# Kernel tuning notes

Measured on AMD Instinct MI355X. Metric: run time of the kernel, lower is better.

## Reference

```python
import jax, jax.numpy as jnp
import numpy as np

INPUT_SIZE = 3072
CORE_SIZE = 1024
OUTPUT_SIZE = 100
BATCH = 8192


def _ri(key, shape, lo, hi):
    # small-range int8 values (torch rand*scale cast to int8)
    return jax.random.randint(key, shape, lo, hi, dtype=jnp.int32).astype(jnp.int8)


def setup_inputs() -> dict:
    key = jax.random.key(0)
    ks = jax.random.split(key, 14)
    return {
        # learned int8 weights (nonzero after EQI.apply updates)
        "W_itoc": _ri(ks[0], (INPUT_SIZE, CORE_SIZE), -3, 4),
        "W_itoc_b": _ri(ks[1], (CORE_SIZE,), -3, 4),
        "W_ctoc": _ri(ks[2], (CORE_SIZE, CORE_SIZE), -3, 4),
        "W_ctoc_b": _ri(ks[3], (CORE_SIZE,), -3, 4),
        "W_ctoo": _ri(ks[4], (CORE_SIZE, OUTPUT_SIZE), -3, 4),
        "W_ctoo_b": _ri(ks[5], (OUTPUT_SIZE,), -3, 4),
        # epsilon perturbations: EPSILON_SCALE=2 -> values in {-1,0,1}
        "e_itoc": _ri(ks[6], (INPUT_SIZE, CORE_SIZE), -2, 2),
        "e_itoc_b": _ri(ks[7], (CORE_SIZE,), -2, 2),
        "e_ctoc": _ri(ks[8], (CORE_SIZE, CORE_SIZE), -2, 2),
        "e_ctoc_b": _ri(ks[9], (CORE_SIZE,), -2, 2),
        "e_ctoo": _ri(ks[10], (CORE_SIZE, OUTPUT_SIZE), -2, 2),
        "e_ctoo_b": _ri(ks[11], (OUTPUT_SIZE,), -2, 2),
        # forward activations
        "inputs": _ri(ks[12], (BATCH, INPUT_SIZE), -4, 5),
        "hiddens": _ri(ks[13], (BATCH, CORE_SIZE), -4, 5),
    }


def _addmm_i8(x, w, b):
    # int8 addmm with wraparound semantics: accumulate in int32, cast back
    # to int8 (truncation == mod-256, matching torch int8 arithmetic).
    acc = jnp.matmul(x.astype(jnp.int32), w.astype(jnp.int32)) + b.astype(jnp.int32)
    return acc.astype(jnp.int8)


def reference(W_itoc, W_itoc_b, W_ctoc, W_ctoc_b, W_ctoo, W_ctoo_b,
              e_itoc, e_itoc_b, e_ctoc, e_ctoc_b, e_ctoo, e_ctoo_b,
              inputs, hiddens):
    # layer 1: inputs -> core (weight = W + epsilon, elementwise int8 add)
    i2c = _addmm_i8(inputs, W_itoc + e_itoc, W_itoc_b + e_itoc_b)      # [B, CORE]
    # layer 2: (hiddens + projected inputs) -> core
    h2 = _addmm_i8(hiddens + i2c, W_ctoc + e_ctoc, W_ctoc_b + e_ctoc_b)  # [B, CORE]
    # layer 3: core -> output
    out = _addmm_i8(h2, W_ctoo + e_ctoo, W_ctoo_b + e_ctoo_b)          # [B, OUT]
    return (h2, out)
```

## Files before the change

### kernel.cpp

```cpp
#include <hip/hip_runtime.h>

typedef int v4i  __attribute__((ext_vector_type(4)));
typedef int v16i __attribute__((ext_vector_type(16)));

__device__ __forceinline__ int pack4i(int a, int b, int c, int d) {
  return (a & 255) | ((b & 255) << 8) | ((c & 255) << 16) | ((d & 255) << 24);
}
__device__ __forceinline__ int badd4(int a, int b) {
  return ((a & 0x7f7f7f7f) + (b & 0x7f7f7f7f)) ^ ((a ^ b) & 0x80808080);
}

__device__ void pack_tile(const int* __restrict__ W, const int* __restrict__ E,
                          char* __restrict__ Bt, int K, int N,
                          int nx, int ky, char* lin) {
  const int t = threadIdx.x;
  const int n0 = nx * 64, k0 = ky * 256;
  {
    const int c  = t & 15;
    const int kq = t >> 4;
    const int ng = n0 + c * 4;
    #pragma unroll 4
    for (int s = 0; s < 16; ++s) {
      const int k = s * 16 + kq;
      const long grow = (long)(k0 + k) * N;
      int a0, a1, a2, a3;
      if (ng + 3 < N) {
        int4 wv = *(const int4*)(W + grow + ng);
        int4 ev = *(const int4*)(E + grow + ng);
        a0 = wv.x + ev.x; a1 = wv.y + ev.y; a2 = wv.z + ev.z; a3 = wv.w + ev.w;
      } else {
        a0 = (ng + 0 < N) ? W[grow + ng + 0] + E[grow + ng + 0] : 0;
        a1 = (ng + 1 < N) ? W[grow + ng + 1] + E[grow + ng + 1] : 0;
        a2 = (ng + 2 < N) ? W[grow + ng + 2] + E[grow + ng + 2] : 0;
        a3 = (ng + 3 < N) ? W[grow + ng + 3] + E[grow + ng + 3] : 0;
      }
      *(int*)(lin + k * 68 + c * 4) = pack4i(a0, a1, a2, a3);
    }
  }
  __syncthreads();
  {
    const int n = t & 63, kq = t >> 6;
    char* dst = Bt + (long)(n0 + n) * K + k0 + (kq << 6);
    int outv[16];
    #pragma unroll
    for (int g = 0; g < 16; ++g) {
      const int k = (kq << 6) + (g << 2);
      outv[g] = pack4i(lin[(k + 0) * 68 + n], lin[(k + 1) * 68 + n],
                       lin[(k + 2) * 68 + n], lin[(k + 3) * 68 + n]);
    }
    #pragma unroll
    for (int g = 0; g < 4; ++g)
      *(int4*)(dst + (g << 4)) =
          make_int4(outv[g * 4], outv[g * 4 + 1], outv[g * 4 + 2], outv[g * 4 + 3]);
  }
}

__global__ __launch_bounds__(256) void pack_weights_kernel(
    const int* W1, const int* E1, char* Bt1,
    const int* W2, const int* E2, char* Bt2,
    const int* W3, const int* E3, char* Bt3,
    const int* b1, const int* eb1, int* bs1,
    const int* b2, const int* eb2, int* bs2,
    const int* b3, const int* eb3, int* bs3) {
  __shared__ __align__(16) char smem[17408];
  const int bid = blockIdx.x;
  if (bid < 192) {
    pack_tile(W1, E1, Bt1, 3072, 1024, bid % 16, bid / 16, smem);
  } else if (bid < 256) {
    const int l = bid - 192;
    pack_tile(W2, E2, Bt2, 1024, 1024, l % 16, l / 16, smem);
  } else if (bid < 264) {
    const int l = bid - 256;
    pack_tile(W3, E3, Bt3, 1024, 100, l & 1, l >> 1, smem);
  } else {
    const int t = threadIdx.x;
    for (int i = t; i < 1024; i += 256) {
      bs1[i] = b1[i] + eb1[i];
      bs2[i] = b2[i] + eb2[i];
    }
    for (int i = t; i < 128; i += 256)
      bs3[i] = (i < 100) ? (b3[i] + eb3[i]) : 0;
  }
}

__global__ __launch_bounds__(256) void pack_copy_kernel(
    const int* __restrict__ X, char* __restrict__ X8,
    const int* __restrict__ H, char* __restrict__ H8) {
  const int bid = blockIdx.x;
  const int t = threadIdx.x;
  const int* __restrict__ src;
  char* __restrict__ dst;
  long base;
  if (bid < 768) { src = X; dst = X8; base = (long)bid * 32768; }
  else           { src = H; dst = H8; base = (long)(bid - 768) * 32768; }
  #pragma unroll 2
  for (int it = 0; it < 8; ++it) {
    const long o = base + (long)it * 4096 + t * 16;
    int4 a = *(const int4*)(src + o);
    int4 b = *(const int4*)(src + o + 4);
    int4 c = *(const int4*)(src + o + 8);
    int4 d = *(const int4*)(src + o + 12);
    *(int4*)(dst + o) = make_int4(pack4i(a.x, a.y, a.z, a.w),
                                  pack4i(b.x, b.y, b.z, b.w),
                                  pack4i(c.x, c.y, c.z, c.w),
                                  pack4i(d.x, d.y, d.z, d.w));
  }
}

template<int EPI>
__global__ __launch_bounds__(256, 4) void gemm_kernel(
    const char* __restrict__ A, const char* __restrict__ Btg,
    const int* __restrict__ bsum, const char* __restrict__ H8,
    char* __restrict__ A8out, int* __restrict__ Iout, const int K) {
  __shared__ __align__(16) char smem[30720];

  const int t = threadIdx.x;
  const int bid = blockIdx.x;
  const int mt = bid & 127, nt = bid >> 7;
  const long m0 = (long)mt << 6;
  const int n0 = nt << 7;

  const int lane = t & 63, w = t >> 6;
  const int lc = lane & 31, hg = lane >> 5;

  v16i acc[2] = {};

  const int am = t >> 2, ah = t & 3;
  const char* Arow = A + (m0 + am) * (long)K + ah * 16;
  const int aoff = am * 80 + ah * 16;
  const int bm = t >> 1, bh = t & 1;
  const char* Brow = Btg + (long)(n0 + bm) * K + bh * 32;
  const int boff = bm * 80 + bh * 32;

  const int abo = lc * 80 + hg * 16;
  const int bbo = (w * 32 + lc) * 80 + hg * 16;

  int4 ar, br0, br1;
  auto LOAD = [&](int kb) {
    ar  = *(const int4*)(Arow + kb);
    br0 = *(const int4*)(Brow + kb);
    br1 = *(const int4*)(Brow + kb + 16);
  };
  auto STORE = [&](int stage) {
    char* base = smem + stage * 15360;
    *(int4*)(base + aoff) = ar;
    *(int4*)(base + 5120 + boff)      = br0;
    *(int4*)(base + 5120 + boff + 16) = br1;
  };

  const int kiters = K >> 6;
  LOAD(0);
  STORE(0);
  __syncthreads();

  for (int kt = 0; kt < kiters; ++kt) {
    if (kt + 1 < kiters) LOAD((kt + 1) << 6);
    const char* base = smem + (kt & 1) * 15360;
    const char* Ab = base + abo;
    const char* Bb = base + 5120 + bbo;
    #pragma unroll
    for (int ks = 0; ks < 2; ++ks) {
      v4i a0 = *(const v4i*)(Ab + ks * 32);
      v4i a1 = *(const v4i*)(Ab + 32 * 80 + ks * 32);
      v4i b  = *(const v4i*)(Bb + ks * 32);
      acc[0] = __builtin_amdgcn_mfma_i32_32x32x32_i8(a0, b, acc[0], 0, 0, 0);
      acc[1] = __builtin_amdgcn_mfma_i32_32x32x32_i8(a1, b, acc[1], 0, 0, 0);
    }
    if (kt + 1 < kiters) {
      STORE((kt + 1) & 1);
      __syncthreads();
    }
  }

  const int gcl = w * 32 + lc;
  const int bs = bsum[n0 + gcl];
  if (EPI == 1) {
    #pragma unroll
    for (int tm = 0; tm < 2; ++tm) {
      #pragma unroll
      for (int r = 0; r < 16; ++r) {
        const int row = tm * 32 + (hg << 2) + (r & 3) + ((r >> 2) << 3);
        Iout[(m0 + row) * 1024 + n0 + gcl] = (int)(signed char)(acc[tm][r] + bs);
      }
    }
  } else {
    __syncthreads();
    #pragma unroll
    for (int tm = 0; tm < 2; ++tm) {
      #pragma unroll
      for (int r = 0; r < 16; ++r) {
        const int row = tm * 32 + (hg << 2) + (r & 3) + ((r >> 2) << 3);
        smem[row * 144 + gcl] = (char)(acc[tm][r] + bs);
      }
    }
    __syncthreads();
    const char* src = smem + (t >> 2) * 144 + (t & 3) * 32;
    const long gm = m0 + (t >> 2);
    const long gco = gm * 1024 + n0 + (t & 3) * 32;
    int4 s0 = *(const int4*)(src);
    int4 s1 = *(const int4*)(src + 16);
    int4 h0 = *(const int4*)(H8 + gco);
    int4 h1 = *(const int4*)(H8 + gco + 16);
    s0 = make_int4(badd4(s0.x, h0.x), badd4(s0.y, h0.y),
                   badd4(s0.z, h0.z), badd4(s0.w, h0.w));
    s1 = make_int4(badd4(s1.x, h1.x), badd4(s1.y, h1.y),
                   badd4(s1.z, h1.z), badd4(s1.w, h1.w));
    *(int4*)(A8out + gco)      = s0;
    *(int4*)(A8out + gco + 16) = s1;
  }
}

__global__ __launch_bounds__(256, 2) void gemm3_kernel(
    const int* __restrict__ h2, const char* __restrict__ Btg,
    const int* __restrict__ bsum, int* __restrict__ Iout) {
  __shared__ __align__(16) char smem[23040];
  const int t = threadIdx.x;
  const int m0 = blockIdx.x << 4;
  const int lane = t & 63, w = t >> 6;
  const int l16 = lane & 15, q = lane >> 4;
  v4i acc0 = {}, acc1 = {};

  const int am = t >> 4, ah = t & 15;
  const int* Arow = h2 + (long)(m0 + am) * 1024 + ah * 4;
  const int aoff = am * 80 + ah * 4;
  const int bm = t >> 1, bh = t & 1;
  const char* Brow = Btg + (long)bm * 1024 + bh * 32;
  const int boff = bm * 80 + bh * 32;

  const int abo  = l16 * 80 + q * 16;
  const int bbo0 = (w * 32 + l16) * 80 + q * 16;
  const int bbo1 = (w * 32 + 16 + l16) * 80 + q * 16;

  int4 ar, br0, br1;
  auto LOAD = [&](int kt) {
    const int kb = kt << 6;
    ar  = *(const int4*)(Arow + kb);
    br0 = *(const int4*)(Brow + kb);
    br1 = *(const int4*)(Brow + kb + 16);
  };
  auto STORE = [&](int stage) {
    char* base = smem + stage * 11520;
    *(int*)(base + aoff) = pack4i(ar.x, ar.y, ar.z, ar.w);
    *(int4*)(base + 1280 + boff)      = br0;
    *(int4*)(base + 1280 + boff + 16) = br1;
  };
  auto MFMA = [&](int stage) {
    const char* base = smem + stage * 11520;
    v4i a  = *(const v4i*)(base + abo);
    v4i b0 = *(const v4i*)(base + 1280 + bbo0);
    v4i b1 = *(const v4i*)(base + 1280 + bbo1);
    acc0 = __builtin_amdgcn_mfma_i32_16x16x64_i8(a, b0, acc0, 0, 0, 0);
    acc1 = __builtin_amdgcn_mfma_i32_16x16x64_i8(a, b1, acc1, 0, 0, 0);
  };

  LOAD(0); STORE(0); __syncthreads();
  for (int kt = 0; kt < 16; ++kt) {
    if (kt + 1 < 16) LOAD(kt + 1);
    MFMA(kt & 1);
    if (kt + 1 < 16) { STORE((kt + 1) & 1); __syncthreads(); }
  }

  const int c0 = w * 32 + l16;
  const int c1 = c0 + 16;
  if (c0 < 100) {
    const int b = bsum[c0];
    #pragma unroll
    for (int r = 0; r < 4; ++r)
      Iout[(long)(m0 + q * 4 + r) * 100 + c0] = (int)(signed char)(acc0[r] + b);
  }
  if (c1 < 100) {
    const int b = bsum[c1];
    #pragma unroll
    for (int r = 0; r < 4; ++r)
      Iout[(long)(m0 + q * 4 + r) * 100 + c1] = (int)(signed char)(acc1[r] + b);
  }
}

extern "C" void kernel_launch(void* const* d_in, const int* in_sizes, int n_in,
                              void* d_out, int out_size, void* d_ws, size_t ws_size,
                              hipStream_t stream) {
  (void)in_sizes; (void)n_in; (void)out_size; (void)ws_size;
  const int* W1  = (const int*)d_in[0];
  const int* b1  = (const int*)d_in[1];
  const int* W2  = (const int*)d_in[2];
  const int* b2  = (const int*)d_in[3];
  const int* W3  = (const int*)d_in[4];
  const int* b3  = (const int*)d_in[5];
  const int* E1  = (const int*)d_in[6];
  const int* eb1 = (const int*)d_in[7];
  const int* E2  = (const int*)d_in[8];
  const int* eb2 = (const int*)d_in[9];
  const int* E3  = (const int*)d_in[10];
  const int* eb3 = (const int*)d_in[11];
  const int* X   = (const int*)d_in[12];
  const int* H   = (const int*)d_in[13];
  int* out = (int*)d_out;

  char* ws  = (char*)d_ws;
  char* Bt1 = ws;
  char* Bt2 = Bt1 + 3145728;
  char* Bt3 = Bt2 + 1048576;
  int*  bs1 = (int*)(Bt3 + 131072);
  int*  bs2 = bs1 + 1024;
  int*  bs3 = bs2 + 1024;
  char* A2  = (char*)(bs3 + 128);
  char* X8  = (char*)d_out;
  char* H8  = X8 + 25165824;

  pack_weights_kernel<<<dim3(265), dim3(256), 0, stream>>>(
      W1, E1, Bt1, W2, E2, Bt2, W3, E3, Bt3,
      b1, eb1, bs1, b2, eb2, bs2, b3, eb3, bs3);

  pack_copy_kernel<<<dim3(1024), dim3(256), 0, stream>>>(X, X8, H, H8);

  gemm_kernel<0><<<dim3(1024), dim3(256), 0, stream>>>(
      X8, Bt1, bs1, H8, A2, nullptr, 3072);

  gemm_kernel<1><<<dim3(1024), dim3(256), 0, stream>>>(
      A2, Bt2, bs2, nullptr, nullptr, out, 1024);

  gemm3_kernel<<<dim3(512), dim3(256), 0, stream>>>(
      out, Bt3, bs3, out + 8388608);
}
```

Before: 312.9 us.

## Fuse int32-to-int8 activation packing into first GEMM and its epilogue

Removes the standalone pass that converted the int32 input and hidden activations to int8. The first GEMM now loads int32 X tiles, packs them into int8 while staging to shared memory, and packs H in the epilogue before the byte-wise add. This saves one kernel launch and the write and reread of the packed copies. In exchange, each X tile is fetched as int32 by every n-tile block, which quadruples A-operand bytes through the cache hierarchy and adds packing ALU work to the main loop.

Result: slower. 339.6 us (+8.6%).

```diff
diff --git a/kernel.cpp b/kernel.cpp
--- a/kernel.cpp
+++ b/kernel.cpp
@@ -83,35 +83,121 @@
   }
 }
 
-__global__ __launch_bounds__(256) void pack_copy_kernel(
-    const int* __restrict__ X, char* __restrict__ X8,
-    const int* __restrict__ H, char* __restrict__ H8) {
+__global__ __launch_bounds__(256, 4) void gemm1_kernel(
+    const int* __restrict__ X, const char* __restrict__ Btg,
+    const int* __restrict__ bsum, const int* __restrict__ H,
+    char* __restrict__ A8out) {
+  const int K = 3072;
+  __shared__ __align__(16) char smem[30720];
+
+  const int t = threadIdx.x;
   const int bid = blockIdx.x;
-  const int t = threadIdx.x;
-  const int* __restrict__ src;
-  char* __restrict__ dst;
-  long base;
-  if (bid < 768) { src = X; dst = X8; base = (long)bid * 32768; }
-  else           { src = H; dst = H8; base = (long)(bid - 768) * 32768; }
-  #pragma unroll 2
-  for (int it = 0; it < 8; ++it) {
-    const long o = base + (long)it * 4096 + t * 16;
-    int4 a = *(const int4*)(src + o);
-    int4 b = *(const int4*)(src + o + 4);
-    int4 c = *(const int4*)(src + o + 8);
-    int4 d = *(const int4*)(src + o + 12);
-    *(int4*)(dst + o) = make_int4(pack4i(a.x, a.y, a.z, a.w),
-                                  pack4i(b.x, b.y, b.z, b.w),
-                                  pack4i(c.x, c.y, c.z, c.w),
-                                  pack4i(d.x, d.y, d.z, d.w));
-  }
-}
-
-template<int EPI>
-__global__ __launch_bounds__(256, 4) void gemm_kernel(
+  const int mt = bid & 127, nt = bid >> 7;
+  const long m0 = (long)mt << 6;
+  const int n0 = nt << 7;
+
+  const int lane = t & 63, w = t >> 6;
+  const int lc = lane & 31, hg = lane >> 5;
+
+  v16i acc[2] = {};
+
+  const int am = t >> 2, ah = t & 3;
+  const int* Xrow = X + (m0 + am) * (long)K + ah * 16;
+  const int aoff = am * 80 + ah * 16;
+  const int bm = t >> 1, bh = t & 1;
+  const char* Brow = Btg + (long)(n0 + bm) * K + bh * 32;
+  const int boff = bm * 80 + bh * 32;
+
+  const int abo = lc * 80 + hg * 16;
+  const int bbo = (w * 32 + lc) * 80 + hg * 16;
+
+  int4 a0r, a1r, a2r, a3r, br0, br1;
+  auto LOAD = [&](int kb) {
+    const int* p = Xrow + kb;
+    a0r = *(const int4*)(p);
+    a1r = *(const int4*)(p + 4);
+    a2r = *(const int4*)(p + 8);
+    a3r = *(const int4*)(p + 12);
+    br0 = *(const int4*)(Brow + kb);
+    br1 = *(const int4*)(Brow + kb + 16);
+  };
+  auto STORE = [&](int stage) {
+    char* base = smem + stage * 15360;
+    *(int4*)(base + aoff) = make_int4(
+        pack4i(a0r.x, a0r.y, a0r.z, a0r.w),
+        pack4i(a1r.x, a1r.y, a1r.z, a1r.w),
+        pack4i(a2r.x, a2r.y, a2r.z, a2r.w),
+        pack4i(a3r.x, a3r.y, a3r.z, a3r.w));
+    *(int4*)(base + 5120 + boff)      = br0;
+    *(int4*)(base + 5120 + boff + 16) = br1;
+  };
+
+  const int kiters = K >> 6;
+  LOAD(0);
+  STORE(0);
+  __syncthreads();
+
+  for (int kt = 0; kt < kiters; ++kt) {
+    if (kt + 1 < kiters) LOAD((kt + 1) << 6);
+    const char* base = smem + (kt & 1) * 15360;
+    const char* Ab = base + abo;
+    const char* Bb = base + 5120 + bbo;
+    #pragma unroll
+    for (int ks = 0; ks < 2; ++ks) {
+      v4i a0 = *(const v4i*)(Ab + ks * 32);
+      v4i a1 = *(const v4i*)(Ab + 32 * 80 + ks * 32);
+      v4i b  = *(const v4i*)(Bb + ks * 32);
+      acc[0] = __builtin_amdgcn_mfma_i32_32x32x32_i8(a0, b, acc[0], 0, 0, 0);
+      acc[1] = __builtin_amdgcn_mfma_i32_32x32x32_i8(a1, b, acc[1], 0, 0, 0);
+    }
+    if (kt + 1 < kiters) {
+      STORE((kt + 1) & 1);
+      __syncthreads();
+    }
+  }
+
+  const int gcl = w * 32 + lc;
+  const int bs = bsum[n0 + gcl];
+  __syncthreads();
+  #pragma unroll
+  for (int tm = 0; tm < 2; ++tm) {
+    #pragma unroll
+    for (int r = 0; r < 16; ++r) {
+      const int row = tm * 32 + (hg << 2) + (r & 3) + ((r >> 2) << 3);
+      smem[row * 144 + gcl] = (char)(acc[tm][r] + bs);
+    }
+  }
+  __syncthreads();
+  const char* src = smem + (t >> 2) * 144 + (t & 3) * 32;
+  const long gm = m0 + (t >> 2);
+  const long gco = gm * 1024 + n0 + (t & 3) * 32;
+  const int* hp = H + gco;
+  int4 s0 = *(const int4*)(src);
+  int4 s1 = *(const int4*)(src + 16);
+  int4 h0 = *(const int4*)(hp);
+  int4 h1 = *(const int4*)(hp + 4);
+  int4 h2 = *(const int4*)(hp + 8);
+  int4 h3 = *(const int4*)(hp + 12);
+  int4 h4 = *(const int4*)(hp + 16);
+  int4 h5 = *(const int4*)(hp + 20);
+  int4 h6 = *(const int4*)(hp + 24);
+  int4 h7 = *(const int4*)(hp + 28);
+  s0 = make_int4(badd4(s0.x, pack4i(h0.x, h0.y, h0.z, h0.w)),
+                 badd4(s0.y, pack4i(h1.x, h1.y, h1.z, h1.w)),
+                 badd4(s0.z, pack4i(h2.x, h2.y, h2.z, h2.w)),
+                 badd4(s0.w, pack4i(h3.x, h3.y, h3.z, h3.w)));
+  s1 = make_int4(badd4(s1.x, pack4i(h4.x, h4.y, h4.z, h4.w)),
+                 badd4(s1.y, pack4i(h5.x, h5.y, h5.z, h5.w)),
+                 badd4(s1.z, pack4i(h6.x, h6.y, h6.z, h6.w)),
+                 badd4(s1.w, pack4i(h7.x, h7.y, h7.z, h7.w)));
+  *(int4*)(A8out + gco)      = s0;
+  *(int4*)(A8out + gco + 16) = s1;
+}
+
+__global__ __launch_bounds__(256, 4) void gemm2_kernel(
     const char* __restrict__ A, const char* __restrict__ Btg,
-    const int* __restrict__ bsum, const char* __restrict__ H8,
-    char* __restrict__ A8out, int* __restrict__ Iout, const int K) {
+    const int* __restrict__ bsum, int* __restrict__ Iout) {
+  const int K = 1024;
   __shared__ __align__(16) char smem[30720];
 
   const int t = threadIdx.x;
@@ -174,39 +260,13 @@
 
   const int gcl = w * 32 + lc;
   const int bs = bsum[n0 + gcl];
-  if (EPI == 1) {
-    #pragma unroll
-    for (int tm = 0; tm < 2; ++tm) {
-      #pragma unroll
-      for (int r = 0; r < 16; ++r) {
-        const int row = tm * 32 + (hg << 2) + (r & 3) + ((r >> 2) << 3);
-        Iout[(m0 + row) * 1024 + n0 + gcl] = (int)(signed char)(acc[tm][r] + bs);
-      }
-    }
-  } else {
-    __syncthreads();
-    #pragma unroll
-    for (int tm = 0; tm < 2; ++tm) {
-      #pragma unroll
-      for (int r = 0; r < 16; ++r) {
-        const int row = tm * 32 + (hg << 2) + (r & 3) + ((r >> 2) << 3);
-        smem[row * 144 + gcl] = (char)(acc[tm][r] + bs);
-      }
-    }
-    __syncthreads();
-    const char* src = smem + (t >> 2) * 144 + (t & 3) * 32;
-    const long gm = m0 + (t >> 2);
-    const long gco = gm * 1024 + n0 + (t & 3) * 32;
-    int4 s0 = *(const int4*)(src);
-    int4 s1 = *(const int4*)(src + 16);
-    int4 h0 = *(const int4*)(H8 + gco);
-    int4 h1 = *(const int4*)(H8 + gco + 16);
-    s0 = make_int4(badd4(s0.x, h0.x), badd4(s0.y, h0.y),
-                   badd4(s0.z, h0.z), badd4(s0.w, h0.w));
-    s1 = make_int4(badd4(s1.x, h1.x), badd4(s1.y, h1.y),
-                   badd4(s1.z, h1.z), badd4(s1.w, h1.w));
-    *(int4*)(A8out + gco)      = s0;
-    *(int4*)(A8out + gco + 16) = s1;
+  #pragma unroll
+  for (int tm = 0; tm < 2; ++tm) {
+    #pragma unroll
+    for (int r = 0; r < 16; ++r) {
+      const int row = tm * 32 + (hg << 2) + (r & 3) + ((r >> 2) << 3);
+      Iout[(m0 + row) * 1024 + n0 + gcl] = (int)(signed char)(acc[tm][r] + bs);
+    }
   }
 }
 
@@ -304,20 +364,14 @@
   int*  bs2 = bs1 + 1024;
   int*  bs3 = bs2 + 1024;
   char* A2  = (char*)(bs3 + 128);
-  char* X8  = (char*)d_out;
-  char* H8  = X8 + 25165824;
 
   pack_weights_kernel<<<dim3(265), dim3(256), 0, stream>>>(
       W1, E1, Bt1, W2, E2, Bt2, W3, E3, Bt3,
       b1, eb1, bs1, b2, eb2, bs2, b3, eb3, bs3);
 
-  pack_copy_kernel<<<dim3(1024), dim3(256), 0, stream>>>(X, X8, H, H8);
-
-  gemm_kernel<0><<<dim3(1024), dim3(256), 0, stream>>>(
-      X8, Bt1, bs1, H8, A2, nullptr, 3072);
-
-  gemm_kernel<1><<<dim3(1024), dim3(256), 0, stream>>>(
-      A2, Bt2, bs2, nullptr, nullptr, out, 1024);
+  gemm1_kernel<<<dim3(1024), dim3(256), 0, stream>>>(X, Bt1, bs1, H, A2);
+
+  gemm2_kernel<<<dim3(1024), dim3(256), 0, stream>>>(A2, Bt2, bs2, out);
 
   gemm3_kernel<<<dim3(512), dim3(256), 0, stream>>>(
       out, Bt3, bs3, out + 8388608);
```

## Fuse int32-to-int8 input packing into GEMM1 and enlarge GEMM tiles to 128x256

Applied to the files above, without the earlier changes.

Removes the separate pack_copy kernel: GEMM1 now reads the int32 inputs directly and packs them to int8 while staging to shared memory, and packs the int32 hiddens in its epilogue. Both large GEMMs switch to 512-thread blocks with 128x256 output tiles (2x2 MFMA per wave) and a two-register-set prefetch scheme. This saves one full pass writing and re-reading packed activations and raises per-block data reuse. In exchange GEMM1 reads 4x more bytes of A per K-step from global memory, and the grid shrinks to 256 blocks, which may underfill the 256 CUs with 2 blocks per CU allowed.

Measured after the change: 310.6 us. No clear change (-0.7%).

```diff
diff --git a/kernel.cpp b/kernel.cpp
--- a/kernel.cpp
+++ b/kernel.cpp
@@ -83,130 +83,218 @@
   }
 }
 
-__global__ __launch_bounds__(256) void pack_copy_kernel(
-    const int* __restrict__ X, char* __restrict__ X8,
-    const int* __restrict__ H, char* __restrict__ H8) {
-  const int bid = blockIdx.x;
-  const int t = threadIdx.x;
-  const int* __restrict__ src;
-  char* __restrict__ dst;
-  long base;
-  if (bid < 768) { src = X; dst = X8; base = (long)bid * 32768; }
-  else           { src = H; dst = H8; base = (long)(bid - 768) * 32768; }
-  #pragma unroll 2
-  for (int it = 0; it < 8; ++it) {
-    const long o = base + (long)it * 4096 + t * 16;
-    int4 a = *(const int4*)(src + o);
-    int4 b = *(const int4*)(src + o + 4);
-    int4 c = *(const int4*)(src + o + 8);
-    int4 d = *(const int4*)(src + o + 12);
-    *(int4*)(dst + o) = make_int4(pack4i(a.x, a.y, a.z, a.w),
-                                  pack4i(b.x, b.y, b.z, b.w),
-                                  pack4i(c.x, c.y, c.z, c.w),
-                                  pack4i(d.x, d.y, d.z, d.w));
-  }
-}
-
-template<int EPI>
-__global__ __launch_bounds__(256, 4) void gemm_kernel(
-    const char* __restrict__ A, const char* __restrict__ Btg,
-    const int* __restrict__ bsum, const char* __restrict__ H8,
-    char* __restrict__ A8out, int* __restrict__ Iout, const int K) {
-  __shared__ __align__(16) char smem[30720];
-
+#define MFMA_I8(a, b, c) __builtin_amdgcn_mfma_i32_32x32x32_i8(a, b, c, 0, 0, 0)
+
+__global__ __launch_bounds__(512, 2) void gemm1_kernel(
+    const int* __restrict__ X, const char* __restrict__ Btg,
+    const int* __restrict__ bsum, const int* __restrict__ H,
+    char* __restrict__ A8out) {
+  const int K = 3072;
+  __shared__ __align__(16) char smem[61440];
   const int t = threadIdx.x;
   const int bid = blockIdx.x;
-  const int mt = bid & 127, nt = bid >> 7;
-  const long m0 = (long)mt << 6;
-  const int n0 = nt << 7;
+  const int mt = bid & 63, nt = bid >> 6;
+  const long m0 = (long)mt << 7;
+  const int n0 = nt << 8;
 
   const int lane = t & 63, w = t >> 6;
   const int lc = lane & 31, hg = lane >> 5;
-
-  v16i acc[2] = {};
-
-  const int am = t >> 2, ah = t & 3;
-  const char* Arow = A + (m0 + am) * (long)K + ah * 16;
-  const int aoff = am * 80 + ah * 16;
-  const int bm = t >> 1, bh = t & 1;
-  const char* Brow = Btg + (long)(n0 + bm) * K + bh * 32;
-  const int boff = bm * 80 + bh * 32;
-
-  const int abo = lc * 80 + hg * 16;
-  const int bbo = (w * 32 + lc) * 80 + hg * 16;
-
-  int4 ar, br0, br1;
-  auto LOAD = [&](int kb) {
-    ar  = *(const int4*)(Arow + kb);
-    br0 = *(const int4*)(Brow + kb);
-    br1 = *(const int4*)(Brow + kb + 16);
+  const int wm = w >> 2, wn = w & 3;
+
+  v16i acc[2][2] = {};
+
+  const int arow = t >> 2, aq = t & 3;
+  const int* Xrow = X + (m0 + arow) * (long)K + aq * 16;
+  const int aoff = arow * 80 + aq * 16;
+  const int brow = t >> 1, bh = t & 1;
+  const char* Brow = Btg + (long)(n0 + brow) * K + bh * 32;
+  const int boff = 10240 + brow * 80 + bh * 32;
+
+  const int aro = (wm * 64 + lc) * 80 + hg * 16;
+  const int bro = 10240 + (wn * 64 + lc) * 80 + hg * 16;
+
+  int4 xa0, xa1, xa2, xa3, xb0, xb1;
+  int4 ya0, ya1, ya2, ya3, yb0, yb1;
+
+#define G1_LOAD(p0,p1,p2,p3,p4,p5,kt) do {                        \
+    const int kb_ = (kt) << 6;                                    \
+    const int* p_ = Xrow + kb_;                                   \
+    p0 = *(const int4*)(p_);      p1 = *(const int4*)(p_ + 4);    \
+    p2 = *(const int4*)(p_ + 8);  p3 = *(const int4*)(p_ + 12);   \
+    p4 = *(const int4*)(Brow + kb_);                              \
+    p5 = *(const int4*)(Brow + kb_ + 16);                         \
+  } while (0)
+#define G1_STORE(p0,p1,p2,p3,p4,p5,stage) do {                    \
+    char* base_ = smem + (stage) * 30720;                         \
+    *(int4*)(base_ + aoff) = make_int4(                           \
+        pack4i(p0.x,p0.y,p0.z,p0.w), pack4i(p1.x,p1.y,p1.z,p1.w), \
+        pack4i(p2.x,p2.y,p2.z,p2.w), pack4i(p3.x,p3.y,p3.z,p3.w));\
+    *(int4*)(base_ + boff)      = p4;                             \
+    *(int4*)(base_ + boff + 16) = p5;                             \
+  } while (0)
+
+  auto MFMA_STEP = [&](int stage) {
+    const char* base = smem + stage * 30720;
+    #pragma unroll
+    for (int ks = 0; ks < 2; ++ks) {
+      v4i a0 = *(const v4i*)(base + aro + ks * 32);
+      v4i a1 = *(const v4i*)(base + aro + 32 * 80 + ks * 32);
+      v4i b0 = *(const v4i*)(base + bro + ks * 32);
+      v4i b1 = *(const v4i*)(base + bro + 32 * 80 + ks * 32);
+      acc[0][0] = MFMA_I8(a0, b0, acc[0][0]);
+      acc[0][1] = MFMA_I8(a0, b1, acc[0][1]);
+      acc[1][0] = MFMA_I8(a1, b0, acc[1][0]);
+      acc[1][1] = MFMA_I8(a1, b1, acc[1][1]);
+    }
   };
-  auto STORE = [&](int stage) {
-    char* base = smem + stage * 15360;
-    *(int4*)(base + aoff) = ar;
-    *(int4*)(base + 5120 + boff)      = br0;
-    *(int4*)(base + 5120 + boff + 16) = br1;
-  };
-
-  const int kiters = K >> 6;
-  LOAD(0);
-  STORE(0);
+
+  const int KIT = K >> 6;
+  G1_LOAD(xa0, xa1, xa2, xa3, xb0, xb1, 0);
+  G1_LOAD(ya0, ya1, ya2, ya3, yb0, yb1, 1);
+  G1_STORE(xa0, xa1, xa2, xa3, xb0, xb1, 0);
   __syncthreads();
 
-  for (int kt = 0; kt < kiters; ++kt) {
-    if (kt + 1 < kiters) LOAD((kt + 1) << 6);
-    const char* base = smem + (kt & 1) * 15360;
-    const char* Ab = base + abo;
-    const char* Bb = base + 5120 + bbo;
-    #pragma unroll
-    for (int ks = 0; ks < 2; ++ks) {
-      v4i a0 = *(const v4i*)(Ab + ks * 32);
-      v4i a1 = *(const v4i*)(Ab + 32 * 80 + ks * 32);
-      v4i b  = *(const v4i*)(Bb + ks * 32);
-      acc[0] = __builtin_amdgcn_mfma_i32_32x32x32_i8(a0, b, acc[0], 0, 0, 0);
-      acc[1] = __builtin_amdgcn_mfma_i32_32x32x32_i8(a1, b, acc[1], 0, 0, 0);
-    }
-    if (kt + 1 < kiters) {
-      STORE((kt + 1) & 1);
+  for (int kt = 0; kt < KIT; kt += 2) {
+    if (kt + 2 < KIT) G1_LOAD(xa0, xa1, xa2, xa3, xb0, xb1, kt + 2);
+    MFMA_STEP(0);
+    G1_STORE(ya0, ya1, ya2, ya3, yb0, yb1, 1);
+    __syncthreads();
+    if (kt + 3 < KIT) G1_LOAD(ya0, ya1, ya2, ya3, yb0, yb1, kt + 3);
+    MFMA_STEP(1);
+    if (kt + 2 < KIT) {
+      G1_STORE(xa0, xa1, xa2, xa3, xb0, xb1, 0);
       __syncthreads();
     }
   }
 
-  const int gcl = w * 32 + lc;
-  const int bs = bsum[n0 + gcl];
-  if (EPI == 1) {
-    #pragma unroll
-    for (int tm = 0; tm < 2; ++tm) {
+  __syncthreads();
+  const int bsj0 = bsum[n0 + wn * 64 + lc];
+  const int bsj1 = bsum[n0 + wn * 64 + 32 + lc];
+  #pragma unroll
+  for (int i = 0; i < 2; ++i) {
+    #pragma unroll
+    for (int j = 0; j < 2; ++j) {
+      const int bsv = j ? bsj1 : bsj0;
+      const int col = wn * 64 + j * 32 + lc;
       #pragma unroll
       for (int r = 0; r < 16; ++r) {
-        const int row = tm * 32 + (hg << 2) + (r & 3) + ((r >> 2) << 3);
-        Iout[(m0 + row) * 1024 + n0 + gcl] = (int)(signed char)(acc[tm][r] + bs);
+        const int row = wm * 64 + i * 32 + (hg << 2) + (r & 3) + ((r >> 2) << 3);
+        smem[row * 272 + col] = (char)(acc[i][j][r] + bsv);
       }
     }
-  } else {
+  }
+  __syncthreads();
+  const int erow = t >> 2, seg = t & 3;
+  const char* src = smem + erow * 272 + seg * 64;
+  const long gm = m0 + erow;
+  const long gco = gm * 1024 + n0 + seg * 64;
+  const int* hp = H + gco;
+  #pragma unroll
+  for (int g = 0; g < 4; ++g) {
+    int4 s  = *(const int4*)(src + g * 16);
+    int4 h0 = *(const int4*)(hp + g * 16);
+    int4 h1 = *(const int4*)(hp + g * 16 + 4);
+    int4 h2 = *(const int4*)(hp + g * 16 + 8);
+    int4 h3 = *(const int4*)(hp + g * 16 + 12);
+    s = make_int4(badd4(s.x, pack4i(h0.x, h0.y, h0.z, h0.w)),
+                  badd4(s.y, pack4i(h1.x, h1.y, h1.z, h1.w)),
+                  badd4(s.z, pack4i(h2.x, h2.y, h2.z, h2.w)),
+                  badd4(s.w, pack4i(h3.x, h3.y, h3.z, h3.w)));
+    *(int4*)(A8out + gco + g * 16) = s;
+  }
+}
+
+__global__ __launch_bounds__(512, 2) void gemm2_kernel(
+    const char* __restrict__ A, const char* __restrict__ Btg,
+    const int* __restrict__ bsum, int* __restrict__ Iout) {
+  const int K = 1024;
+  __shared__ __align__(16) char smem[61440];
+  const int t = threadIdx.x;
+  const int bid = blockIdx.x;
+  const int mt = bid & 63, nt = bid >> 6;
+  const long m0 = (long)mt << 7;
+  const int n0 = nt << 8;
+
+  const int lane = t & 63, w = t >> 6;
+  const int lc = lane & 31, hg = lane >> 5;
+  const int wm = w >> 2, wn = w & 3;
+
+  v16i acc[2][2] = {};
+
+  const int arow = t >> 2, aq = t & 3;
+  const char* Arow = A + (m0 + arow) * (long)K + aq * 16;
+  const int aoff = arow * 80 + aq * 16;
+  const int brow = t >> 1, bh = t & 1;
+  const char* Brow = Btg + (long)(n0 + brow) * K + bh * 32;
+  const int boff = 10240 + brow * 80 + bh * 32;
+
+  const int aro = (wm * 64 + lc) * 80 + hg * 16;
+  const int bro = 10240 + (wn * 64 + lc) * 80 + hg * 16;
+
+  int4 xa0, xb0, xb1;
+  int4 ya0, yb0, yb1;
+
+#define G2_LOAD(p0,p4,p5,kt) do {                                 \
+    const int kb_ = (kt) << 6;                                    \
+    p0 = *(const int4*)(Arow + kb_);                              \
+    p4 = *(const int4*)(Brow + kb_);                              \
+    p5 = *(const int4*)(Brow + kb_ + 16);                         \
+  } while (0)
+#define G2_STORE(p0,p4,p5,stage) do {                             \
+    char* base_ = smem + (stage) * 30720;                         \
+    *(int4*)(base_ + aoff)      = p0;                             \
+    *(int4*)(base_ + boff)      = p4;                             \
+    *(int4*)(base_ + boff + 16) = p5;                             \
+  } while (0)
+
+  auto MFMA_STEP = [&](int stage) {
+    const char* base = smem + stage * 30720;
+    #pragma unroll
+    for (int ks = 0; ks < 2; ++ks) {
+      v4i a0 = *(const v4i*)(base + aro + ks * 32);
+      v4i a1 = *(const v4i*)(base + aro + 32 * 80 + ks * 32);
+      v4i b0 = *(const v4i*)(base + bro + ks * 32);
+      v4i b1 = *(const v4i*)(base + bro + 32 * 80 + ks * 32);
+      acc[0][0] = MFMA_I8(a0, b0, acc[0][0]);
+      acc[0][1] = MFMA_I8(a0, b1, acc[0][1]);
+      acc[1][0] = MFMA_I8(a1, b0, acc[1][0]);
+      acc[1][1] = MFMA_I8(a1, b1, acc[1][1]);
+    }
+  };
+
+  const int KIT = K >> 6;
+  G2_LOAD(xa0, xb0, xb1, 0);
+  G2_LOAD(ya0, yb0, yb1, 1);
+  G2_STORE(xa0, xb0, xb1, 0);
+  __syncthreads();
+
+  for (int kt = 0; kt < KIT; kt += 2) {
+    if (kt + 2 < KIT) G2_LOAD(xa0, xb0, xb1, kt + 2);
+    MFMA_STEP(0);
+    G2_STORE(ya0, yb0, yb1, 1);
     __syncthreads();
-    #pragma unroll
-    for (int tm = 0; tm < 2; ++tm) {
+    if (kt + 3 < KIT) G2_LOAD(ya0, yb0, yb1, kt + 3);
+    MFMA_STEP(1);
+    if (kt + 2 < KIT) {
+      G2_STORE(xa0, xb0, xb1, 0);
+      __syncthreads();
+    }
+  }
+
+  const int bsj0 = bsum[n0 + wn * 64 + lc];
+  const int bsj1 = bsum[n0 + wn * 64 + 32 + lc];
+  #pragma unroll
+  for (int i = 0; i < 2; ++i) {
+    #pragma unroll
+    for (int j = 0; j < 2; ++j) {
+      const int bsv = j ? bsj1 : bsj0;
+      const int col = n0 + wn * 64 + j * 32 + lc;
       #pragma unroll
       for (int r = 0; r < 16; ++r) {
-        const int row = tm * 32 + (hg << 2) + (r & 3) + ((r >> 2) << 3);
-        smem[row * 144 + gcl] = (char)(acc[tm][r] + bs);
+        const long row = m0 + wm * 64 + i * 32 + (hg << 2) + (r & 3) + ((r >> 2) << 3);
+        Iout[row * 1024 + col] = (int)(signed char)(acc[i][j][r] + bsv);
       }
     }
-    __syncthreads();
-    const char* src = smem + (t >> 2) * 144 + (t & 3) * 32;
-    const long gm = m0 + (t >> 2);
-    const long gco = gm * 1024 + n0 + (t & 3) * 32;
-    int4 s0 = *(const int4*)(src);
-    int4 s1 = *(const int4*)(src + 16);
-    int4 h0 = *(const int4*)(H8 + gco);
-    int4 h1 = *(const int4*)(H8 + gco + 16);
-    s0 = make_int4(badd4(s0.x, h0.x), badd4(s0.y, h0.y),
-                   badd4(s0.z, h0.z), badd4(s0.w, h0.w));
-    s1 = make_int4(badd4(s1.x, h1.x), badd4(s1.y, h1.y),
-                   badd4(s1.z, h1.z), badd4(s1.w, h1.w));
-    *(int4*)(A8out + gco)      = s0;
-    *(int4*)(A8out + gco + 16) = s1;
   }
 }
 
@@ -304,20 +392,14 @@
   int*  bs2 = bs1 + 1024;
   int*  bs3 = bs2 + 1024;
   char* A2  = (char*)(bs3 + 128);
-  char* X8  = (char*)d_out;
-  char* H8  = X8 + 25165824;
 
   pack_weights_kernel<<<dim3(265), dim3(256), 0, stream>>>(
       W1, E1, Bt1, W2, E2, Bt2, W3, E3, Bt3,
       b1, eb1, bs1, b2, eb2, bs2, b3, eb3, bs3);
 
-  pack_copy_kernel<<<dim3(1024), dim3(256), 0, stream>>>(X, X8, H, H8);
-
-  gemm_kernel<0><<<dim3(1024), dim3(256), 0, stream>>>(
-      X8, Bt1, bs1, H8, A2, nullptr, 3072);
-
-  gemm_kernel<1><<<dim3(1024), dim3(256), 0, stream>>>(
-      A2, Bt2, bs2, nullptr, nullptr, out, 1024);
+  gemm1_kernel<<<dim3(256), dim3(512), 0, stream>>>(X, Bt1, bs1, H, A2);
+
+  gemm2_kernel<<<dim3(256), dim3(512), 0, stream>>>(A2, Bt2, bs2, out);
 
   gemm3_kernel<<<dim3(512), dim3(256), 0, stream>>>(
       out, Bt3, bs3, out + 8388608);
```
